# Kernel tuning notes

Measured on AMD Instinct MI355X. Metric: run time of the kernel, lower is better.

## Reference

```python
import jax, jax.numpy as jnp
import numpy as np

DIM, HID, SEQ = 768, 2048, 4096
LR, MOM, WD, THRESH = 1e-3, 0.9, 0.01, 0.1


def _net(p, x):
    W1, b1, W2, b2, W3, b3, W4, b4 = p
    h = jax.nn.relu(x @ W1 + b1)
    h = jax.nn.relu(h @ W2 + b2)
    h = jax.nn.relu(h @ W3 + b3)
    return h @ W4 + b4


def _loss(p, t):
    # t: [dim]; token.unsqueeze(0) then mse_loss (mean over all elements)
    pred = _net(p, t[None, :])
    return jnp.mean((pred - t[None, :]) ** 2)


def _ttt(params, x):
    toks = x[::4]  # `if i % 4 != 0: continue`

    def step(carry, t):
        p, buf, inited = carry
        g = jax.grad(_loss)(p, t)
        surprise = sum(jnp.linalg.norm(gi) for gi in jax.tree_util.tree_leaves(g))
        # momentum buffer: first observation initializes it
        buf_new = jnp.where(inited, MOM * buf + (1.0 - MOM) * surprise, surprise)

        def upd(q):
            qd = jax.tree_util.tree_map(lambda w: w * (1.0 - WD), q)  # weight decay
            g2 = jax.grad(_loss)(qd, t)                                # fresh fwd/bwd
            return jax.tree_util.tree_map(lambda w, gi: w - LR * gi, qd, g2)  # SGD step

        p_new = jax.lax.cond(buf_new > THRESH, upd, lambda q: q, p)
        return (p_new, buf_new, jnp.bool_(True)), None

    (pf, _, _), _ = jax.lax.scan(step, (params, jnp.float32(0.0), jnp.bool_(False)), toks)
    return pf


def setup_inputs() -> dict:
    key = jax.random.key(0)
    ks = jax.random.split(key, 5)

    def lin(k, fi, fo):
        kw, kb = jax.random.split(k)
        w = jax.random.normal(kw, (fi, fo), jnp.float32) / np.sqrt(fi).astype(np.float32)
        b = jax.random.normal(kb, (fo,), jnp.float32) * 0.01
        return w, b

    W1, b1 = lin(ks[0], DIM, HID)
    W2, b2 = lin(ks[1], HID, HID)
    W3, b3 = lin(ks[2], HID, HID)
    W4, b4 = lin(ks[3], HID, DIM)
    x = jax.random.normal(ks[4], (SEQ, DIM), jnp.float32)
    return dict(x=x, W1=W1, b1=b1, W2=W2, b2=b2, W3=W3, b3=b3, W4=W4, b4=b4, do_ttt=1)


def reference(x, W1, b1, W2, b2, W3, b3, W4, b4, do_ttt):
    params = (W1, b1, W2, b2, W3, b3, W4, b4)
    if do_ttt:
        params = _ttt(params, x)
    out = _net(params, x)            # eval pass over full sequence
    return out.mean(axis=0, keepdims=True)  # memory_summary [1, dim]
```

## Files before the change

### kernel.cpp

```cpp
#include <hip/hip_runtime.h>
#include <cstddef>

#define LRC 0.001f
#define DEC 0.99f

typedef float f32x4 __attribute__((ext_vector_type(4)));

static const size_t OFF_H1F = 376832;
static const size_t OFF_H2F = 380928;
static const size_t OFF_H2Q = 382976;
static const size_t OFF_H3F = 385024;
static const size_t OFF_H3Q = 387072;
static const size_t OFF_D4F = 389120;
static const size_t OFF_D4Q = 389888;
static const size_t OFF_D3F = 390656;
static const size_t OFF_D3Q = 392704;
static const size_t OFF_D2F = 394752;
static const size_t OFF_D2Q = 396800;
static const size_t OFF_SL4 = 398848;
static const size_t OFF_D1Q = 400896;
static const size_t OFF_NSQ = 402944;
static const size_t OFF_SL3 = 402960;
static const size_t OFF_SL2 = 403216;
static const size_t OFF_SL1 = 403472;
static const size_t OFF_MSUM = 403732;
static const size_t OFF_HA  = 428308;
static const size_t OFF_HB  = 2525460;

#define ST0  0
#define ST1  2048
#define ST2  4096
#define ST3  6144
#define SD4F 8192
#define SD4Q 8960
#define SRED 9728
#define SCND 10240
#define SBUF 10244
#define SCOND 10245
#define SB4  10248
#define SSQ  10256
#define SWRP 10264
#define SWRQ 10288

__device__ __forceinline__ float clf(const float* p) {
    return __hip_atomic_load(p, __ATOMIC_RELAXED, __HIP_MEMORY_SCOPE_AGENT);
}
__device__ __forceinline__ void csf(float* p, float v) {
    __hip_atomic_store(p, v, __ATOMIC_RELAXED, __HIP_MEMORY_SCOPE_AGENT);
}
__device__ __forceinline__ f32x4 cl4(const float* p) {
    f32x4 r;
    asm volatile("global_load_dwordx4 %0, %1, off sc0 sc1" : "=&v"(r) : "v"(p) : "memory");
    return r;
}
__device__ __forceinline__ void cs4(float* p, f32x4 v) {
    asm volatile("global_store_dwordx4 %0, %1, off sc0 sc1" :: "v"(p), "v"(v) : "memory");
}
__device__ __forceinline__ void vwait() {
    asm volatile("s_waitcnt vmcnt(0)" ::: "memory");
    __builtin_amdgcn_sched_barrier(0);
}

__device__ __forceinline__ float dot4(const f32x4 a, const f32x4 b) {
    float s = a.x * b.x; s += a.y * b.y; s += a.z * b.z; s += a.w * b.w; return s;
}
__device__ __forceinline__ int swz(int p) { return p ^ (((p >> 5) & 7) << 2); }

__device__ __forceinline__ void updc(f32x4& wv, const f32x4 a, float dq) {
    wv.x = DEC * wv.x - (LRC * a.x) * dq;
    wv.y = DEC * wv.y - (LRC * a.y) * dq;
    wv.z = DEC * wv.z - (LRC * a.z) * dq;
    wv.w = DEC * wv.w - (LRC * a.w) * dq;
}
__device__ __forceinline__ void updr(f32x4& wv, float u, const f32x4 dv) {
    wv.x = DEC * wv.x - u * dv.x;
    wv.y = DEC * wv.y - u * dv.y;
    wv.z = DEC * wv.z - u * dv.z;
    wv.w = DEC * wv.w - u * dv.w;
}

__device__ __forceinline__ float block_reduce_512s(float v, float* red) {
    int t = threadIdx.x;
    red[t] = v;
    __syncthreads();
    for (int st = 256; st > 0; st >>= 1) {
        if (t < st) red[t] += red[t + st];
        __syncthreads();
    }
    float r = red[0];
    __syncthreads();
    return r;
}

__device__ __forceinline__ void gbar(unsigned* bar) {
    asm volatile("s_waitcnt vmcnt(0) lgkmcnt(0)" ::: "memory");
    __syncthreads();
    if (threadIdx.x == 0) {
        unsigned g = __hip_atomic_load(bar, __ATOMIC_RELAXED, __HIP_MEMORY_SCOPE_AGENT);
        unsigned* grp = bar + 64 + ((blockIdx.x >> 4) << 5);
        bool released = false;
        if (__hip_atomic_fetch_add(grp, 1u, __ATOMIC_RELAXED, __HIP_MEMORY_SCOPE_AGENT) == 15u) {
            if (__hip_atomic_fetch_add(bar + 32, 1u, __ATOMIC_RELAXED, __HIP_MEMORY_SCOPE_AGENT) == 15u) {
#pragma unroll
                for (int i = 0; i < 16; ++i)
                    __hip_atomic_store(bar + 64 + (i << 5), 0u, __ATOMIC_RELAXED, __HIP_MEMORY_SCOPE_AGENT);
                __hip_atomic_store(bar + 32, 0u, __ATOMIC_RELAXED, __HIP_MEMORY_SCOPE_AGENT);
                __hip_atomic_store(bar, g + 1u, __ATOMIC_RELEASE, __HIP_MEMORY_SCOPE_AGENT);
                released = true;
            }
        }
        if (!released) {
            while (__hip_atomic_load(bar, __ATOMIC_RELAXED, __HIP_MEMORY_SCOPE_AGENT) == g)
                __builtin_amdgcn_s_sleep(2);
            (void)__hip_atomic_load(bar, __ATOMIC_ACQUIRE, __HIP_MEMORY_SCOPE_AGENT);
        }
    }
    __syncthreads();
}

__global__ __launch_bounds__(1024) void k_zero(unsigned* __restrict__ bar) {
    bar[threadIdx.x] = 0u;
}

#define L3M(M) M(0) M(1) M(2)
#define L8M(M) M(0) M(1) M(2) M(3) M(4) M(5) M(6) M(7)
#define LDS_SW(buf, i) (*(const f32x4*)(smem + (buf) + swz(32 * lane + 4 * (i))))
#define LDS_D4(buf, i) (*(const f32x4*)(smem + (buf) + 12 * lane + 4 * (i)))

__global__ void __attribute__((amdgpu_flat_work_group_size(512, 512), amdgpu_waves_per_eu(2, 2)))
k_scan(const float* __restrict__ x,
       float* __restrict__ W1g, float* __restrict__ b1g,
       float* __restrict__ W2g, float* __restrict__ b2g,
       float* __restrict__ W3g, float* __restrict__ b3g,
       float* __restrict__ W4g, float* __restrict__ b4g,
       float* __restrict__ wsf,
       const int* __restrict__ flag) {
    if (*flag == 0) return;
    __shared__ __align__(16) float smem[16896];
    unsigned* bar = (unsigned*)(wsf + OFF_HA);
    const int b = blockIdx.x, tid = threadIdx.x;
    const int w = tid >> 6, lane = tid & 63;
    const int jw = 8 * b + w;
    const int c3 = 3 * b;
    const int t4 = tid * 4;

    f32x4 w1c0, w1c1, w1c2;
    f32x4 w2c0, w2c1, w2c2, w2c3, w2c4, w2c5, w2c6, w2c7;
    f32x4 w3c0, w3c1, w3c2, w3c3, w3c4, w3c5, w3c6, w3c7;
    f32x4 w4c0, w4c1, w4c2;
    f32x4 w4r0, w4r1, w4r2;
    f32x4 w2r0, w2r1, w2r2, w2r3, w2r4, w2r5, w2r6, w2r7;
    f32x4 w3r0, w3r1, w3r2, w3r3, w3r4, w3r5, w3r6, w3r7;

#define LD_COL(dst, Wg, ld, row0, col) { f32x4 t; \
    t.x = Wg[(size_t)((row0) + 0) * (ld) + (col)]; \
    t.y = Wg[(size_t)((row0) + 1) * (ld) + (col)]; \
    t.z = Wg[(size_t)((row0) + 2) * (ld) + (col)]; \
    t.w = Wg[(size_t)((row0) + 3) * (ld) + (col)]; dst = t; }
#define LDW1C(i) LD_COL(w1c##i, W1g, 2048, 12 * lane + 4 * (i), jw)
    L3M(LDW1C)
#undef LDW1C
#define LDW2C(i) LD_COL(w2c##i, W2g, 2048, 32 * lane + 4 * (i), jw)
    L8M(LDW2C)
#undef LDW2C
#define LDW3C(i) LD_COL(w3c##i, W3g, 2048, 32 * lane + 4 * (i), jw)
    L8M(LDW3C)
#undef LDW3C
#define LDW4C(i) LD_COL(w4c##i, W4g, 768, 4 * tid, c3 + (i))
    L3M(LDW4C)
#undef LDW4C
#define LDW4R(i) w4r##i = *(const f32x4*)(W4g + (size_t)jw * 768 + 12 * lane + 4 * (i));
    L3M(LDW4R)
#undef LDW4R
#define LDW2R(i) w2r##i = *(const f32x4*)(W2g + (size_t)jw * 2048 + 32 * lane + 4 * (i));
    L8M(LDW2R)
#undef LDW2R
#define LDW3R(i) w3r##i = *(const f32x4*)(W3g + (size_t)jw * 2048 + 32 * lane + 4 * (i));
    L8M(LDW3R)
#undef LDW3R
    if (tid == 0) smem[SBUF] = 0.f;

    for (int s = 0; s < 1024; ++s) {
        const float* xt = x + (size_t)s * 3072;
        const float* xprev = x + (size_t)(s > 0 ? s - 1 : 0) * 3072;

        float cond = 0.f;
        if (s > 0) {
            if (w < 4) {
                const float* sl = wsf + (w == 0 ? OFF_SL1 : w == 1 ? OFF_SL2 : w == 2 ? OFF_SL3 : OFF_SL4);
                float v = clf(sl + lane) + clf(sl + lane + 64) + clf(sl + lane + 128) + clf(sl + lane + 192);
#pragma unroll
                for (int off = 32; off > 0; off >>= 1) v += __shfl_down(v, off);
                if (lane == 0) smem[SCND + w] = v;
            }
            __syncthreads();
            if (tid == 0) {
                float nd1 = sqrtf(smem[SCND + 0]), nd2 = sqrtf(smem[SCND + 1]);
                float nd3 = sqrtf(smem[SCND + 2]), nd4 = sqrtf(smem[SCND + 3]);
                float nx = sqrtf(clf(wsf + OFF_NSQ + 0));
                float nh1 = sqrtf(clf(wsf + OFF_NSQ + 1));
                float nh2 = sqrtf(clf(wsf + OFF_NSQ + 2));
                float nh3 = sqrtf(clf(wsf + OFF_NSQ + 3));
                float surprise = nx * nd1 + nd1 + nh1 * nd2 + nd2 + nh2 * nd3 + nd3 + nh3 * nd4 + nd4;
                float bufold = smem[SBUF];
                float bufnew = (s == 1) ? surprise : (0.9f * bufold + 0.1f * surprise);
                smem[SBUF] = bufnew;
                smem[SCOND] = (bufnew > 0.1f) ? 1.f : 0.f;
            }
            __syncthreads();
            cond = smem[SCOND];
        }
        float b1j;
        if (cond != 0.f) {
            f32x4 a0 = cl4(wsf + OFF_H1F + t4);
            f32x4 a1 = cl4(wsf + OFF_H2Q + t4);
            f32x4 a2 = cl4(wsf + OFF_D2Q + t4);
            f32x4 a3 = cl4(wsf + OFF_D3Q + t4);
            f32x4 hq3 = cl4(wsf + OFF_H3Q + t4);
            f32x4 d4s = {0.f, 0.f, 0.f, 0.f};
            if (tid < 192) d4s = cl4(wsf + OFF_D4Q + t4);
            float d1qj = clf(wsf + OFF_D1Q + jw);
            float h3qr = clf(wsf + OFF_H3Q + jw);
            float h2qr = clf(wsf + OFF_H2Q + jw);
            float ob1 = b1g[jw];
            f32x4 xp0 = *(const f32x4*)(xprev + 12 * lane);
            f32x4 xp1 = *(const f32x4*)(xprev + 12 * lane + 4);
            f32x4 xp2 = *(const f32x4*)(xprev + 12 * lane + 8);
            vwait();
            {
                int st = swz(t4);
                *(f32x4*)(smem + ST0 + st) = a0;
                *(f32x4*)(smem + ST1 + st) = a1;
                *(f32x4*)(smem + ST2 + st) = a2;
                *(f32x4*)(smem + ST3 + st) = a3;
            }
            if (tid < 192) *(f32x4*)(smem + SD4Q + t4) = d4s;
            __syncthreads();
            updc(w1c0, xp0, d1qj); updc(w1c1, xp1, d1qj); updc(w1c2, xp2, d1qj);
            {
                float d2qj = smem[ST2 + swz(jw)];
#define UPW2C(i) { f32x4 hf = LDS_SW(ST0, i); f32x4 af; \
                   af.x = DEC * hf.x; af.y = DEC * hf.y; af.z = DEC * hf.z; af.w = DEC * hf.w; \
                   updc(w2c##i, af, d2qj); }
                L8M(UPW2C)
#undef UPW2C
            }
            {
                float d3qj = smem[ST3 + swz(jw)];
#define UPW3C(i) { f32x4 hq = LDS_SW(ST1, i); updc(w3c##i, hq, d3qj); }
                L8M(UPW3C)
#undef UPW3C
            }
            {
                float vq0 = smem[SD4Q + c3 + 0];
                float vq1 = smem[SD4Q + c3 + 1];
                float vq2 = smem[SD4Q + c3 + 2];
                updc(w4c0, hq3, vq0); updc(w4c1, hq3, vq1); updc(w4c2, hq3, vq2);
            }
            {
                float u = LRC * h3qr;
#define UPW4R(i) { f32x4 dv = LDS_D4(SD4Q, i); updr(w4r##i, u, dv); }
                L3M(UPW4R)
#undef UPW4R
            }
            {
                float u = LRC * h2qr;
#define UPW3R(i) { f32x4 dv = LDS_SW(ST3, i); updr(w3r##i, u, dv); }
                L8M(UPW3R)
#undef UPW3R
            }
            {
                float u = LRC * (DEC * smem[ST0 + swz(jw)]);
#define UPW2R(i) { f32x4 dv = LDS_SW(ST2, i); updr(w2r##i, u, dv); }
                L8M(UPW2R)
#undef UPW2R
            }
            b1j = DEC * ob1 - LRC * d1qj;
            if (lane == 0) b1g[jw] = b1j;
        } else {
            b1j = b1g[jw];
        }
        {
            f32x4 x0 = *(const f32x4*)(xt + 12 * lane);
            f32x4 x1 = *(const f32x4*)(xt + 12 * lane + 4);
            f32x4 x2 = *(const f32x4*)(xt + 12 * lane + 8);
            float acc = dot4(w1c0, x0);
            acc += dot4(w1c1, x1);
            acc += dot4(w1c2, x2);
#pragma unroll
            for (int off = 32; off > 0; off >>= 1) acc += __shfl_down(acc, off);
            if (lane == 0) csf(wsf + OFF_H1F + jw, fmaxf(acc + b1j, 0.f));
        }
        gbar(bar);

        {
            f32x4 hv = cl4(wsf + OFF_H1F + t4);
            float ob2 = b2g[jw];
            float d2qjo = (cond != 0.f) ? clf(wsf + OFF_D2Q + jw) : 0.f;
            vwait();
            *(f32x4*)(smem + ST0 + swz(t4)) = hv;
            float b2j = (cond != 0.f) ? (DEC * ob2 - LRC * d2qjo) : ob2;
            if (cond != 0.f && lane == 0) b2g[jw] = b2j;
            __syncthreads();
            float accP = 0.f, accQ = 0.f;
#define PHB(i) { const f32x4 hf = LDS_SW(ST0, i); f32x4 hq; \
                 hq.x = DEC * hf.x; hq.y = DEC * hf.y; hq.z = DEC * hf.z; hq.w = DEC * hf.w; \
                 accP += dot4(w2c##i, hf); accQ += dot4(w2c##i, hq); }
            L8M(PHB)
#undef PHB
#pragma unroll
            for (int off = 32; off > 0; off >>= 1) {
                accP += __shfl_down(accP, off);
                accQ += __shfl_down(accQ, off);
            }
            if (lane == 0) {
                csf(wsf + OFF_H2F + jw, fmaxf(accP + b2j, 0.f));
                csf(wsf + OFF_H2Q + jw, fmaxf(DEC * (accQ + b2j), 0.f));
            }
        }
        gbar(bar);

        {
            f32x4 hfv = cl4(wsf + OFF_H2F + t4);
            f32x4 hqv = cl4(wsf + OFF_H2Q + t4);
            float ob3 = b3g[jw];
            float d3qjo = (cond != 0.f) ? clf(wsf + OFF_D3Q + jw) : 0.f;
            vwait();
            {
                int st = swz(t4);
                *(f32x4*)(smem + ST0 + st) = hfv;
                *(f32x4*)(smem + ST1 + st) = hqv;
            }
            float b3j = (cond != 0.f) ? (DEC * ob3 - LRC * d3qjo) : ob3;
            if (cond != 0.f && lane == 0) b3g[jw] = b3j;
            __syncthreads();
            float accP = 0.f, accQ = 0.f;
#define PHC(i) { const f32x4 hf = LDS_SW(ST0, i); const f32x4 hq = LDS_SW(ST1, i); \
                 accP += dot4(w3c##i, hf); accQ += dot4(w3c##i, hq); }
            L8M(PHC)
#undef PHC
#pragma unroll
            for (int off = 32; off > 0; off >>= 1) {
                accP += __shfl_down(accP, off);
                accQ += __shfl_down(accQ, off);
            }
            if (lane == 0) {
                csf(wsf + OFF_H3F + jw, fmaxf(accP + b3j, 0.f));
                csf(wsf + OFF_H3Q + jw, fmaxf(DEC * (accQ + b3j), 0.f));
            }
        }
        gbar(bar);

        {
            f32x4 hfv = cl4(wsf + OFF_H3F + t4);
            f32x4 hqv = cl4(wsf + OFF_H3Q + t4);
            float tv = 0.f;
            if (tid < 3) {
                float ob4 = b4g[c3 + tid];
                float d4qjo = (cond != 0.f) ? clf(wsf + OFF_D4Q + c3 + tid) : 0.f;
                tv = xt[c3 + tid];
                float bn = (cond != 0.f) ? (DEC * ob4 - LRC * d4qjo) : ob4;
                if (cond != 0.f) b4g[c3 + tid] = bn;
                smem[SB4 + tid] = bn;
            }
            vwait();
            {
                int st = swz(t4);
                *(f32x4*)(smem + ST0 + st) = hfv;
                *(f32x4*)(smem + ST1 + st) = hqv;
            }
            float aP0 = dot4(w4c0, hfv), aP1 = dot4(w4c1, hfv), aP2 = dot4(w4c2, hfv);
            float aQ0 = dot4(w4c0, hqv), aQ1 = dot4(w4c1, hqv), aQ2 = dot4(w4c2, hqv);
#pragma unroll
            for (int off = 32; off > 0; off >>= 1) {
                aP0 += __shfl_down(aP0, off); aP1 += __shfl_down(aP1, off); aP2 += __shfl_down(aP2, off);
                aQ0 += __shfl_down(aQ0, off); aQ1 += __shfl_down(aQ1, off); aQ2 += __shfl_down(aQ2, off);
            }
            if (lane == 0) {
                smem[SWRP + w * 3 + 0] = aP0; smem[SWRP + w * 3 + 1] = aP1; smem[SWRP + w * 3 + 2] = aP2;
                smem[SWRQ + w * 3 + 0] = aQ0; smem[SWRQ + w * 3 + 1] = aQ1; smem[SWRQ + w * 3 + 2] = aQ2;
            }
            __syncthreads();
            if (tid < 3) {
                float zp = 0.f, zq = 0.f;
#pragma unroll
                for (int q = 0; q < 8; ++q) { zp += smem[SWRP + q * 3 + tid]; zq += smem[SWRQ + q * 3 + tid]; }
                float bn = smem[SB4 + tid];
                float d4f = 2.f * ((zp + bn) - tv) * (1.f / 768.f);
                float d4q = 2.f * (DEC * (zq + bn) - tv) * (1.f / 768.f);
                csf(wsf + OFF_D4F + c3 + tid, d4f);
                csf(wsf + OFF_D4Q + c3 + tid, d4q);
                smem[SSQ + tid] = d4f * d4f;
            }
            __syncthreads();
            if (tid == 0) csf(wsf + OFF_SL4 + b, smem[SSQ + 0] + smem[SSQ + 1] + smem[SSQ + 2]);
            if (b >= 1 && b <= 4) {
                float v = 0.f;
                if (b == 4) {
                    if (tid < 192) {
                        f32x4 xv = *(const f32x4*)(xt + t4);
                        v = xv.x * xv.x + xv.y * xv.y + xv.z * xv.z + xv.w * xv.w;
                    }
                } else {
                    const float* src = (b == 1) ? wsf + OFF_H1F : (b == 2) ? wsf + OFF_H2F : wsf + OFF_H3F;
                    f32x4 hh = cl4(src + t4);
                    vwait();
                    v = hh.x * hh.x + hh.y * hh.y + hh.z * hh.z + hh.w * hh.w;
                }
                float sres = block_reduce_512s(v, smem + SRED);
                if (tid == 0) csf(wsf + OFF_NSQ + ((b == 4) ? 0 : b), sres);
            }
        }
        gbar(bar);

        {
            f32x4 p4 = {0.f, 0.f, 0.f, 0.f}, q4 = {0.f, 0.f, 0.f, 0.f};
            if (tid < 192) {
                p4 = cl4(wsf + OFF_D4F + t4);
                q4 = cl4(wsf + OFF_D4Q + t4);
            }
            vwait();
            if (tid < 192) {
                *(f32x4*)(smem + SD4F + t4) = p4;
                *(f32x4*)(smem + SD4Q + t4) = q4;
            }
            __syncthreads();
            float accP = 0.f, accQ = 0.f;
#define PHE(i) { const f32x4 dP = LDS_D4(SD4F, i); const f32x4 dQ = LDS_D4(SD4Q, i); \
                 accP += dot4(w4r##i, dP); accQ += dot4(w4r##i, dQ); }
            L3M(PHE)
#undef PHE
#pragma unroll
            for (int off = 32; off > 0; off >>= 1) {
                accP += __shfl_down(accP, off);
                accQ += __shfl_down(accQ, off);
            }
            if (lane == 0) {
                float dp = (smem[ST0 + swz(jw)] > 0.f) ? accP : 0.f;
                float dq = (smem[ST1 + swz(jw)] > 0.f) ? DEC * accQ : 0.f;
                csf(wsf + OFF_D3F + jw, dp);
                csf(wsf + OFF_D3Q + jw, dq);
                smem[SSQ + w] = dp * dp;
            }
            __syncthreads();
            if (tid == 0) {
                float ss = 0.f;
#pragma unroll
                for (int q = 0; q < 8; ++q) ss += smem[SSQ + q];
                csf(wsf + OFF_SL3 + b, ss);
            }
        }
        gbar(bar);

        {
            f32x4 fP = cl4(wsf + OFF_D3F + t4);
            f32x4 fQ = cl4(wsf + OFF_D3Q + t4);
            float h2fr = clf(wsf + OFF_H2F + jw);
            float h2qr = clf(wsf + OFF_H2Q + jw);
            vwait();
            {
                int st = swz(t4);
                *(f32x4*)(smem + ST2 + st) = fP;
                *(f32x4*)(smem + ST3 + st) = fQ;
            }
            __syncthreads();
            float accP = 0.f, accQ = 0.f;
#define PHF(i) { const f32x4 dP = LDS_SW(ST2, i); const f32x4 dQ = LDS_SW(ST3, i); \
                 accP += dot4(w3r##i, dP); accQ += dot4(w3r##i, dQ); }
            L8M(PHF)
#undef PHF
#pragma unroll
            for (int off = 32; off > 0; off >>= 1) {
                accP += __shfl_down(accP, off);
                accQ += __shfl_down(accQ, off);
            }
            if (lane == 0) {
                float dp = (h2fr > 0.f) ? accP : 0.f;
                float dq = (h2qr > 0.f) ? DEC * accQ : 0.f;
                csf(wsf + OFF_D2F + jw, dp);
                csf(wsf + OFF_D2Q + jw, dq);
                smem[SSQ + w] = dp * dp;
            }
            __syncthreads();
            if (tid == 0) {
                float ss = 0.f;
#pragma unroll
                for (int q = 0; q < 8; ++q) ss += smem[SSQ + q];
                csf(wsf + OFF_SL2 + b, ss);
            }
        }
        gbar(bar);

        {
            f32x4 fP = cl4(wsf + OFF_D2F + t4);
            f32x4 fQ = cl4(wsf + OFF_D2Q + t4);
            float h1fr = clf(wsf + OFF_H1F + jw);
            vwait();
            {
                int st = swz(t4);
                *(f32x4*)(smem + ST0 + st) = fP;
                *(f32x4*)(smem + ST1 + st) = fQ;
            }
            __syncthreads();
            float accP = 0.f, accQ = 0.f;
#define PHG(i) { const f32x4 dP = LDS_SW(ST0, i); const f32x4 dQ = LDS_SW(ST1, i); \
                 accP += dot4(w2r##i, dP); accQ += dot4(w2r##i, dQ); }
            L8M(PHG)
#undef PHG
#pragma unroll
            for (int off = 32; off > 0; off >>= 1) {
                accP += __shfl_down(accP, off);
                accQ += __shfl_down(accQ, off);
            }
            if (lane == 0) {
                float dp = (h1fr > 0.f) ? accP : 0.f;
                float h1qr = DEC * h1fr;
                float dq = (h1qr > 0.f) ? DEC * accQ : 0.f;
                csf(wsf + OFF_D1Q + jw, dq);
                smem[SSQ + w] = dp * dp;
            }
            __syncthreads();
            if (tid == 0) {
                float ss = 0.f;
#pragma unroll
                for (int q = 0; q < 8; ++q) ss += smem[SSQ + q];
                csf(wsf + OFF_SL1 + b, ss);
            }
        }
        gbar(bar);
    }

    {
        if (w < 4) {
            const float* sl = wsf + (w == 0 ? OFF_SL1 : w == 1 ? OFF_SL2 : w == 2 ? OFF_SL3 : OFF_SL4);
            float v = clf(sl + lane) + clf(sl + lane + 64) + clf(sl + lane + 128) + clf(sl + lane + 192);
#pragma unroll
            for (int off = 32; off > 0; off >>= 1) v += __shfl_down(v, off);
            if (lane == 0) smem[SCND + w] = v;
        }
        __syncthreads();
        if (tid == 0) {
            float nd1 = sqrtf(smem[SCND + 0]), nd2 = sqrtf(smem[SCND + 1]);
            float nd3 = sqrtf(smem[SCND + 2]), nd4 = sqrtf(smem[SCND + 3]);
            float nx = sqrtf(clf(wsf + OFF_NSQ + 0));
            float nh1 = sqrtf(clf(wsf + OFF_NSQ + 1));
            float nh2 = sqrtf(clf(wsf + OFF_NSQ + 2));
            float nh3 = sqrtf(clf(wsf + OFF_NSQ + 3));
            float surprise = nx * nd1 + nd1 + nh1 * nd2 + nd2 + nh2 * nd3 + nd3 + nh3 * nd4 + nd4;
            float bufnew = 0.9f * smem[SBUF] + 0.1f * surprise;
            smem[SCOND] = (bufnew > 0.1f) ? 1.f : 0.f;
        }
        __syncthreads();
        if (smem[SCOND] != 0.f) {
            const float* xpE = x + (size_t)1023 * 3072;
            f32x4 a0 = cl4(wsf + OFF_H1F + t4);
            f32x4 a1 = cl4(wsf + OFF_H2Q + t4);
            f32x4 hq3 = cl4(wsf + OFF_H3Q + t4);
            f32x4 d4s = {0.f, 0.f, 0.f, 0.f};
            if (tid < 192) d4s = cl4(wsf + OFF_D4Q + t4);
            float d1qj = clf(wsf + OFF_D1Q + jw);
            float d2qj = clf(wsf + OFF_D2Q + jw);
            float d3qj = clf(wsf + OFF_D3Q + jw);
            f32x4 xp0 = *(const f32x4*)(xpE + 12 * lane);
            f32x4 xp1 = *(const f32x4*)(xpE + 12 * lane + 4);
            f32x4 xp2 = *(const f32x4*)(xpE + 12 * lane + 8);
            vwait();
            {
                int st = swz(t4);
                *(f32x4*)(smem + ST0 + st) = a0;
                *(f32x4*)(smem + ST1 + st) = a1;
            }
            if (tid < 192) *(f32x4*)(smem + SD4Q + t4) = d4s;
            __syncthreads();
            updc(w1c0, xp0, d1qj); updc(w1c1, xp1, d1qj); updc(w1c2, xp2, d1qj);
#define EPW2C(i) { f32x4 hf = LDS_SW(ST0, i); f32x4 af; \
                   af.x = DEC * hf.x; af.y = DEC * hf.y; af.z = DEC * hf.z; af.w = DEC * hf.w; \
                   updc(w2c##i, af, d2qj); }
            L8M(EPW2C)
#undef EPW2C
#define EPW3C(i) { f32x4 hq = LDS_SW(ST1, i); updc(w3c##i, hq, d3qj); }
            L8M(EPW3C)
#undef EPW3C
            {
                float vq0 = smem[SD4Q + c3 + 0];
                float vq1 = smem[SD4Q + c3 + 1];
                float vq2 = smem[SD4Q + c3 + 2];
                updc(w4c0, hq3, vq0); updc(w4c1, hq3, vq1); updc(w4c2, hq3, vq2);
            }
            if (lane == 0) {
                b1g[jw] = DEC * b1g[jw] - LRC * d1qj;
                b2g[jw] = DEC * b2g[jw] - LRC * d2qj;
                b3g[jw] = DEC * b3g[jw] - LRC * d3qj;
            }
            if (tid < 3) b4g[c3 + tid] = DEC * b4g[c3 + tid] - LRC * smem[SD4Q + c3 + tid];
        }
    }

    __syncthreads();
    {
#define WBW2(i) { smem[(32 * lane + 4 * (i) + 0) * 8 + w] = w2c##i.x; \
                  smem[(32 * lane + 4 * (i) + 1) * 8 + w] = w2c##i.y; \
                  smem[(32 * lane + 4 * (i) + 2) * 8 + w] = w2c##i.z; \
                  smem[(32 * lane + 4 * (i) + 3) * 8 + w] = w2c##i.w; }
        L8M(WBW2)
#undef WBW2
        __syncthreads();
#pragma unroll
        for (int r2 = 0; r2 < 4; ++r2) {
            int r = t4 + r2;
            *(f32x4*)(W2g + (size_t)r * 2048 + 8 * b) = *(const f32x4*)(smem + r * 8);
            *(f32x4*)(W2g + (size_t)r * 2048 + 8 * b + 4) = *(const f32x4*)(smem + r * 8 + 4);
        }
        __syncthreads();
    }
    {
#define WBW3(i) { smem[(32 * lane + 4 * (i) + 0) * 8 + w] = w3c##i.x; \
                  smem[(32 * lane + 4 * (i) + 1) * 8 + w] = w3c##i.y; \
                  smem[(32 * lane + 4 * (i) + 2) * 8 + w] = w3c##i.z; \
                  smem[(32 * lane + 4 * (i) + 3) * 8 + w] = w3c##i.w; }
        L8M(WBW3)
#undef WBW3
        __syncthreads();
#pragma unroll
        for (int r2 = 0; r2 < 4; ++r2) {
            int r = t4 + r2;
            *(f32x4*)(W3g + (size_t)r * 2048 + 8 * b) = *(const f32x4*)(smem + r * 8);
            *(f32x4*)(W3g + (size_t)r * 2048 + 8 * b + 4) = *(const f32x4*)(smem + r * 8 + 4);
        }
        __syncthreads();
    }
    {
#define WBW1(i) { smem[(12 * lane + 4 * (i) + 0) * 8 + w] = w1c##i.x; \
                  smem[(12 * lane + 4 * (i) + 1) * 8 + w] = w1c##i.y; \
                  smem[(12 * lane + 4 * (i) + 2) * 8 + w] = w1c##i.z; \
                  smem[(12 * lane + 4 * (i) + 3) * 8 + w] = w1c##i.w; }
        L3M(WBW1)
#undef WBW1
        __syncthreads();
        for (int r = tid; r < 768; r += 512) {
            *(f32x4*)(W1g + (size_t)r * 2048 + 8 * b) = *(const f32x4*)(smem + r * 8);
            *(f32x4*)(W1g + (size_t)r * 2048 + 8 * b + 4) = *(const f32x4*)(smem + r * 8 + 4);
        }
        __syncthreads();
    }
    {
#define WBW4(c) { smem[(4 * tid + 0) * 3 + (c)] = w4c##c.x; \
                  smem[(4 * tid + 1) * 3 + (c)] = w4c##c.y; \
                  smem[(4 * tid + 2) * 3 + (c)] = w4c##c.z; \
                  smem[(4 * tid + 3) * 3 + (c)] = w4c##c.w; }
        L3M(WBW4)
#undef WBW4
        __syncthreads();
#pragma unroll
        for (int r2 = 0; r2 < 4; ++r2) {
            int r = t4 + r2;
            W4g[(size_t)r * 768 + c3 + 0] = smem[r * 3 + 0];
            W4g[(size_t)r * 768 + c3 + 1] = smem[r * 3 + 1];
            W4g[(size_t)r * 768 + c3 + 2] = smem[r * 3 + 2];
        }
    }
}

__global__ __launch_bounds__(256) void k_gemm(const float* __restrict__ A,
                                              const float* __restrict__ W,
                                              const float* __restrict__ bias,
                                              float* __restrict__ C,
                                              int M, int N, int K, int do_relu) {
    __shared__ float sA[16][64];
    __shared__ float sB[16][128];
    int bn = blockIdx.x, bm = blockIdx.y;
    int m0 = bm * 64, n0 = bn * 128;
    int tid = threadIdx.x;
    int tx = tid & 31, ty = tid >> 5;
    float acc[8][4];
#pragma unroll
    for (int i = 0; i < 8; ++i)
#pragma unroll
        for (int j = 0; j < 4; ++j) acc[i][j] = 0.f;

// ... 94 lines not shown
```

Baseline: 66.14 ms.

## Replicate published cross-block vectors into 8 copies to spread coherent reads

Every value a block publishes for other blocks (activations, deltas, norms, partial sums) is now written to 8 replica regions, and each block reads from the replica chosen by its block index mod 8. The aim is to spread the many coherent, cache-bypassing loads that all 256 blocks issue against the same small addresses after each grid barrier, reducing hot-spot contention on the same L2/memory channels. In exchange every publish costs 8 stores, and the barrier now waits for outstanding stores before arriving. The replicas reuse the workspace region at OFF_HB, which assumes that area is otherwise unused during the scan.

```diff
diff --git a/kernel.cpp b/kernel.cpp
--- a/kernel.cpp
+++ b/kernel.cpp
@@ -26,6 +26,7 @@
 static const size_t OFF_MSUM = 403732;
 static const size_t OFF_HA  = 428308;
 static const size_t OFF_HB  = 2525460;
+static const size_t OFF_STG = 2525460;
 
 #define ST0  0
 #define ST1  2048
@@ -53,12 +54,17 @@
     asm volatile("global_load_dwordx4 %0, %1, off sc0 sc1" : "=&v"(r) : "v"(p) : "memory");
     return r;
 }
-__device__ __forceinline__ void cs4(float* p, f32x4 v) {
-    asm volatile("global_store_dwordx4 %0, %1, off sc0 sc1" :: "v"(p), "v"(v) : "memory");
-}
 __device__ __forceinline__ void vwait() {
     asm volatile("s_waitcnt vmcnt(0)" ::: "memory");
     __builtin_amdgcn_sched_barrier(0);
+}
+
+__device__ __forceinline__ float* repb(float* wsf, int r) {
+    return (r == 0) ? wsf : (wsf + (OFF_STG - OFF_H1F) + (size_t)(r - 1) * 32768);
+}
+__device__ __forceinline__ void pubf(float* wsf, size_t off, float v) {
+#pragma unroll
+    for (int r = 0; r < 8; ++r) csf(repb(wsf, r) + off, v);
 }
 
 __device__ __forceinline__ float dot4(const f32x4 a, const f32x4 b) {
@@ -97,6 +103,7 @@
     __syncthreads();
     if (threadIdx.x == 0) {
         unsigned g = __hip_atomic_load(bar, __ATOMIC_RELAXED, __HIP_MEMORY_SCOPE_AGENT);
+        asm volatile("s_waitcnt vmcnt(0)" ::: "memory");
         unsigned* grp = bar + 64 + ((blockIdx.x >> 4) << 5);
         bool released = false;
         if (__hip_atomic_fetch_add(grp, 1u, __ATOMIC_RELAXED, __HIP_MEMORY_SCOPE_AGENT) == 15u) {
@@ -127,14 +134,14 @@
 #define LDS_SW(buf, i) (*(const f32x4*)(smem + (buf) + swz(32 * lane + 4 * (i))))
 #define LDS_D4(buf, i) (*(const f32x4*)(smem + (buf) + 12 * lane + 4 * (i)))
 
-__global__ void __attribute__((amdgpu_flat_work_group_size(512, 512), amdgpu_waves_per_eu(2, 2)))
-k_scan(const float* __restrict__ x,
-       float* __restrict__ W1g, float* __restrict__ b1g,
-       float* __restrict__ W2g, float* __restrict__ b2g,
-       float* __restrict__ W3g, float* __restrict__ b3g,
-       float* __restrict__ W4g, float* __restrict__ b4g,
-       float* __restrict__ wsf,
-       const int* __restrict__ flag) {
+__global__ __attribute__((amdgpu_flat_work_group_size(512, 512), amdgpu_waves_per_eu(2, 2)))
+void k_scan(const float* __restrict__ x,
+            float* __restrict__ W1g, float* __restrict__ b1g,
+            float* __restrict__ W2g, float* __restrict__ b2g,
+            float* __restrict__ W3g, float* __restrict__ b3g,
+            float* __restrict__ W4g, float* __restrict__ b4g,
+            float* __restrict__ wsf,
+            const int* __restrict__ flag) {
     if (*flag == 0) return;
     __shared__ __align__(16) float smem[16896];
     unsigned* bar = (unsigned*)(wsf + OFF_HA);
@@ -143,6 +150,7 @@
     const int jw = 8 * b + w;
     const int c3 = 3 * b;
     const int t4 = tid * 4;
+    float* rb = repb(wsf, b & 7);
 
     f32x4 w1c0, w1c1, w1c2;
     f32x4 w2c0, w2c1, w2c2, w2c3, w2c4, w2c5, w2c6, w2c7;
@@ -187,7 +195,7 @@
         float cond = 0.f;
         if (s > 0) {
             if (w < 4) {
-                const float* sl = wsf + (w == 0 ? OFF_SL1 : w == 1 ? OFF_SL2 : w == 2 ? OFF_SL3 : OFF_SL4);
+                const float* sl = rb + (w == 0 ? OFF_SL1 : w == 1 ? OFF_SL2 : w == 2 ? OFF_SL3 : OFF_SL4);
                 float v = clf(sl + lane) + clf(sl + lane + 64) + clf(sl + lane + 128) + clf(sl + lane + 192);
 #pragma unroll
                 for (int off = 32; off > 0; off >>= 1) v += __shfl_down(v, off);
@@ -197,10 +205,10 @@
             if (tid == 0) {
                 float nd1 = sqrtf(smem[SCND + 0]), nd2 = sqrtf(smem[SCND + 1]);
                 float nd3 = sqrtf(smem[SCND + 2]), nd4 = sqrtf(smem[SCND + 3]);
-                float nx = sqrtf(clf(wsf + OFF_NSQ + 0));
-                float nh1 = sqrtf(clf(wsf + OFF_NSQ + 1));
-                float nh2 = sqrtf(clf(wsf + OFF_NSQ + 2));
-                float nh3 = sqrtf(clf(wsf + OFF_NSQ + 3));
+                float nx = sqrtf(clf(rb + OFF_NSQ + 0));
+                float nh1 = sqrtf(clf(rb + OFF_NSQ + 1));
+                float nh2 = sqrtf(clf(rb + OFF_NSQ + 2));
+                float nh3 = sqrtf(clf(rb + OFF_NSQ + 3));
                 float surprise = nx * nd1 + nd1 + nh1 * nd2 + nd2 + nh2 * nd3 + nd3 + nh3 * nd4 + nd4;
                 float bufold = smem[SBUF];
                 float bufnew = (s == 1) ? surprise : (0.9f * bufold + 0.1f * surprise);
@@ -212,16 +220,16 @@
         }
         float b1j;
         if (cond != 0.f) {
-            f32x4 a0 = cl4(wsf + OFF_H1F + t4);
-            f32x4 a1 = cl4(wsf + OFF_H2Q + t4);
-            f32x4 a2 = cl4(wsf + OFF_D2Q + t4);
-            f32x4 a3 = cl4(wsf + OFF_D3Q + t4);
-            f32x4 hq3 = cl4(wsf + OFF_H3Q + t4);
+            f32x4 a0 = cl4(rb + OFF_H1F + t4);
+            f32x4 a1 = cl4(rb + OFF_H2Q + t4);
+            f32x4 a2 = cl4(rb + OFF_D2Q + t4);
+            f32x4 a3 = cl4(rb + OFF_D3Q + t4);
+            f32x4 hq3 = cl4(rb + OFF_H3Q + t4);
             f32x4 d4s = {0.f, 0.f, 0.f, 0.f};
-            if (tid < 192) d4s = cl4(wsf + OFF_D4Q + t4);
-            float d1qj = clf(wsf + OFF_D1Q + jw);
-            float h3qr = clf(wsf + OFF_H3Q + jw);
-            float h2qr = clf(wsf + OFF_H2Q + jw);
+            if (tid < 192) d4s = cl4(rb + OFF_D4Q + t4);
+            float d1qj = clf(rb + OFF_D1Q + jw);
+            float h3qr = clf(rb + OFF_H3Q + jw);
+            float h2qr = clf(rb + OFF_H2Q + jw);
             float ob1 = b1g[jw];
             f32x4 xp0 = *(const f32x4*)(xprev + 12 * lane);
             f32x4 xp1 = *(const f32x4*)(xprev + 12 * lane + 4);
@@ -289,14 +297,14 @@
             acc += dot4(w1c2, x2);
 #pragma unroll
             for (int off = 32; off > 0; off >>= 1) acc += __shfl_down(acc, off);
-            if (lane == 0) csf(wsf + OFF_H1F + jw, fmaxf(acc + b1j, 0.f));
+            if (lane == 0) pubf(wsf, OFF_H1F + jw, fmaxf(acc + b1j, 0.f));
         }
         gbar(bar);
 
         {
-            f32x4 hv = cl4(wsf + OFF_H1F + t4);
+            f32x4 hv = cl4(rb + OFF_H1F + t4);
             float ob2 = b2g[jw];
-            float d2qjo = (cond != 0.f) ? clf(wsf + OFF_D2Q + jw) : 0.f;
+            float d2qjo = (cond != 0.f) ? clf(rb + OFF_D2Q + jw) : 0.f;
             vwait();
             *(f32x4*)(smem + ST0 + swz(t4)) = hv;
             float b2j = (cond != 0.f) ? (DEC * ob2 - LRC * d2qjo) : ob2;
@@ -314,17 +322,17 @@
                 accQ += __shfl_down(accQ, off);
             }
             if (lane == 0) {
-                csf(wsf + OFF_H2F + jw, fmaxf(accP + b2j, 0.f));
-                csf(wsf + OFF_H2Q + jw, fmaxf(DEC * (accQ + b2j), 0.f));
+                pubf(wsf, OFF_H2F + jw, fmaxf(accP + b2j, 0.f));
+                pubf(wsf, OFF_H2Q + jw, fmaxf(DEC * (accQ + b2j), 0.f));
             }
         }
         gbar(bar);
 
         {
-            f32x4 hfv = cl4(wsf + OFF_H2F + t4);
-            f32x4 hqv = cl4(wsf + OFF_H2Q + t4);
+            f32x4 hfv = cl4(rb + OFF_H2F + t4);
+            f32x4 hqv = cl4(rb + OFF_H2Q + t4);
             float ob3 = b3g[jw];
-            float d3qjo = (cond != 0.f) ? clf(wsf + OFF_D3Q + jw) : 0.f;
+            float d3qjo = (cond != 0.f) ? clf(rb + OFF_D3Q + jw) : 0.f;
             vwait();
             {
                 int st = swz(t4);
@@ -345,19 +353,19 @@
                 accQ += __shfl_down(accQ, off);
             }
             if (lane == 0) {
-                csf(wsf + OFF_H3F + jw, fmaxf(accP + b3j, 0.f));
-                csf(wsf + OFF_H3Q + jw, fmaxf(DEC * (accQ + b3j), 0.f));
+                pubf(wsf, OFF_H3F + jw, fmaxf(accP + b3j, 0.f));
+                pubf(wsf, OFF_H3Q + jw, fmaxf(DEC * (accQ + b3j), 0.f));
             }
         }
         gbar(bar);
 
         {
-            f32x4 hfv = cl4(wsf + OFF_H3F + t4);
-            f32x4 hqv = cl4(wsf + OFF_H3Q + t4);
+            f32x4 hfv = cl4(rb + OFF_H3F + t4);
+            f32x4 hqv = cl4(rb + OFF_H3Q + t4);
             float tv = 0.f;
             if (tid < 3) {
                 float ob4 = b4g[c3 + tid];
-                float d4qjo = (cond != 0.f) ? clf(wsf + OFF_D4Q + c3 + tid) : 0.f;
+                float d4qjo = (cond != 0.f) ? clf(rb + OFF_D4Q + c3 + tid) : 0.f;
                 tv = xt[c3 + tid];
                 float bn = (cond != 0.f) ? (DEC * ob4 - LRC * d4qjo) : ob4;
                 if (cond != 0.f) b4g[c3 + tid] = bn;
@@ -388,12 +396,12 @@
                 float bn = smem[SB4 + tid];
                 float d4f = 2.f * ((zp + bn) - tv) * (1.f / 768.f);
                 float d4q = 2.f * (DEC * (zq + bn) - tv) * (1.f / 768.f);
-                csf(wsf + OFF_D4F + c3 + tid, d4f);
-                csf(wsf + OFF_D4Q + c3 + tid, d4q);
+                pubf(wsf, OFF_D4F + c3 + tid, d4f);
+                pubf(wsf, OFF_D4Q + c3 + tid, d4q);
                 smem[SSQ + tid] = d4f * d4f;
             }
             __syncthreads();
-            if (tid == 0) csf(wsf + OFF_SL4 + b, smem[SSQ + 0] + smem[SSQ + 1] + smem[SSQ + 2]);
+            if (tid == 0) pubf(wsf, OFF_SL4 + b, smem[SSQ + 0] + smem[SSQ + 1] + smem[SSQ + 2]);
             if (b >= 1 && b <= 4) {
                 float v = 0.f;
                 if (b == 4) {
@@ -402,13 +410,13 @@
                         v = xv.x * xv.x + xv.y * xv.y + xv.z * xv.z + xv.w * xv.w;
                     }
                 } else {
-                    const float* src = (b == 1) ? wsf + OFF_H1F : (b == 2) ? wsf + OFF_H2F : wsf + OFF_H3F;
-                    f32x4 hh = cl4(src + t4);
+                    const size_t soff = (b == 1) ? OFF_H1F : (b == 2) ? OFF_H2F : OFF_H3F;
+                    f32x4 hh = cl4(rb + soff + t4);
                     vwait();
                     v = hh.x * hh.x + hh.y * hh.y + hh.z * hh.z + hh.w * hh.w;
                 }
                 float sres = block_reduce_512s(v, smem + SRED);
-                if (tid == 0) csf(wsf + OFF_NSQ + ((b == 4) ? 0 : b), sres);
+                if (tid == 0) pubf(wsf, OFF_NSQ + ((b == 4) ? 0 : b), sres);
             }
         }
         gbar(bar);
@@ -416,8 +424,8 @@
         {
             f32x4 p4 = {0.f, 0.f, 0.f, 0.f}, q4 = {0.f, 0.f, 0.f, 0.f};
             if (tid < 192) {
-                p4 = cl4(wsf + OFF_D4F + t4);
-                q4 = cl4(wsf + OFF_D4Q + t4);
+                p4 = cl4(rb + OFF_D4F + t4);
+                q4 = cl4(rb + OFF_D4Q + t4);
             }
             vwait();
             if (tid < 192) {
@@ -438,8 +446,8 @@
             if (lane == 0) {
                 float dp = (smem[ST0 + swz(jw)] > 0.f) ? accP : 0.f;
                 float dq = (smem[ST1 + swz(jw)] > 0.f) ? DEC * accQ : 0.f;
-                csf(wsf + OFF_D3F + jw, dp);
-                csf(wsf + OFF_D3Q + jw, dq);
+                pubf(wsf, OFF_D3F + jw, dp);
+                pubf(wsf, OFF_D3Q + jw, dq);
                 smem[SSQ + w] = dp * dp;
             }
             __syncthreads();
@@ -447,16 +455,16 @@
                 float ss = 0.f;
 #pragma unroll
                 for (int q = 0; q < 8; ++q) ss += smem[SSQ + q];
-                csf(wsf + OFF_SL3 + b, ss);
+                pubf(wsf, OFF_SL3 + b, ss);
             }
         }
         gbar(bar);
 
         {
-            f32x4 fP = cl4(wsf + OFF_D3F + t4);
-            f32x4 fQ = cl4(wsf + OFF_D3Q + t4);
-            float h2fr = clf(wsf + OFF_H2F + jw);
-            float h2qr = clf(wsf + OFF_H2Q + jw);
+            f32x4 fP = cl4(rb + OFF_D3F + t4);
+            f32x4 fQ = cl4(rb + OFF_D3Q + t4);
+            float h2fr = clf(rb + OFF_H2F + jw);
+            float h2qr = clf(rb + OFF_H2Q + jw);
             vwait();
             {
                 int st = swz(t4);
@@ -477,8 +485,8 @@
             if (lane == 0) {
                 float dp = (h2fr > 0.f) ? accP : 0.f;
                 float dq = (h2qr > 0.f) ? DEC * accQ : 0.f;
-                csf(wsf + OFF_D2F + jw, dp);
-                csf(wsf + OFF_D2Q + jw, dq);
+                pubf(wsf, OFF_D2F + jw, dp);
+                pubf(wsf, OFF_D2Q + jw, dq);
                 smem[SSQ + w] = dp * dp;
             }
             __syncthreads();
@@ -486,15 +494,15 @@
                 float ss = 0.f;
 #pragma unroll
                 for (int q = 0; q < 8; ++q) ss += smem[SSQ + q];
-                csf(wsf + OFF_SL2 + b, ss);
+                pubf(wsf, OFF_SL2 + b, ss);
             }
         }
         gbar(bar);
 
         {
-            f32x4 fP = cl4(wsf + OFF_D2F + t4);
-            f32x4 fQ = cl4(wsf + OFF_D2Q + t4);
-            float h1fr = clf(wsf + OFF_H1F + jw);
+            f32x4 fP = cl4(rb + OFF_D2F + t4);
+            f32x4 fQ = cl4(rb + OFF_D2Q + t4);
+            float h1fr = clf(rb + OFF_H1F + jw);
             vwait();
             {
                 int st = swz(t4);
@@ -516,7 +524,7 @@
                 float dp = (h1fr > 0.f) ? accP : 0.f;
                 float h1qr = DEC * h1fr;
                 float dq = (h1qr > 0.f) ? DEC * accQ : 0.f;
-                csf(wsf + OFF_D1Q + jw, dq);
+                pubf(wsf, OFF_D1Q + jw, dq);
                 smem[SSQ + w] = dp * dp;
             }
             __syncthreads();
@@ -524,7 +532,7 @@
                 float ss = 0.f;
 #pragma unroll
                 for (int q = 0; q < 8; ++q) ss += smem[SSQ + q];
-                csf(wsf + OFF_SL1 + b, ss);
+                pubf(wsf, OFF_SL1 + b, ss);
             }
         }
         gbar(bar);
```

New measurement: 100.2 ms. 1.51x slower.

## Stage cross-block vectors into per-XCD L2 copies with local barriers

Applied to the files above, without the earlier changes.

After each grid barrier, blocks on the same XCD (found via HW_REG_XCC_ID) cooperatively copy the shared activation and delta vectors from coherent global memory into a per-XCD staging area. A local barrier then lets every block read them with sc0-only loads that may hit the local L2, instead of each block doing system-coherent sc0 sc1 loads. The aim is to cut repeated cross-die coherent traffic on every scan step. The cost is an extra copy and an extra per-XCD barrier at each phase, plus reliance on the XCD id mapping and cache semantics for correctness.

```diff
diff --git a/kernel.cpp b/kernel.cpp
--- a/kernel.cpp
+++ b/kernel.cpp
@@ -26,6 +26,7 @@
 static const size_t OFF_MSUM = 403732;
 static const size_t OFF_HA  = 428308;
 static const size_t OFF_HB  = 2525460;
+static const size_t OFF_STG = 2525460;
 
 #define ST0  0
 #define ST1  2048
@@ -53,12 +54,20 @@
     asm volatile("global_load_dwordx4 %0, %1, off sc0 sc1" : "=&v"(r) : "v"(p) : "memory");
     return r;
 }
-__device__ __forceinline__ void cs4(float* p, f32x4 v) {
-    asm volatile("global_store_dwordx4 %0, %1, off sc0 sc1" :: "v"(p), "v"(v) : "memory");
-}
 __device__ __forceinline__ void vwait() {
     asm volatile("s_waitcnt vmcnt(0)" ::: "memory");
     __builtin_amdgcn_sched_barrier(0);
+}
+__device__ __forceinline__ f32x4 s4(const float* p) {
+    f32x4 r;
+    asm volatile("global_load_dwordx4 %0, %1, off sc0" : "=&v"(r) : "v"(p) : "memory");
+    return r;
+}
+__device__ __forceinline__ float s1(const float* p) {
+    float r;
+    asm volatile("global_load_dword %0, %1, off sc0\n\t"
+                 "s_waitcnt vmcnt(0)" : "=&v"(r) : "v"(p) : "memory");
+    return r;
 }
 
 __device__ __forceinline__ float dot4(const f32x4 a, const f32x4 b) {
@@ -97,6 +106,7 @@
     __syncthreads();
     if (threadIdx.x == 0) {
         unsigned g = __hip_atomic_load(bar, __ATOMIC_RELAXED, __HIP_MEMORY_SCOPE_AGENT);
+        asm volatile("s_waitcnt vmcnt(0)" ::: "memory");
         unsigned* grp = bar + 64 + ((blockIdx.x >> 4) << 5);
         bool released = false;
         if (__hip_atomic_fetch_add(grp, 1u, __ATOMIC_RELAXED, __HIP_MEMORY_SCOPE_AGENT) == 15u) {
@@ -118,8 +128,40 @@
     __syncthreads();
 }
 
+__device__ __forceinline__ void lbar(unsigned* lg, unsigned* la, unsigned m) {
+    asm volatile("s_waitcnt vmcnt(0) lgkmcnt(0)" ::: "memory");
+    __syncthreads();
+    if (threadIdx.x == 0) {
+        unsigned g = __hip_atomic_load(lg, __ATOMIC_RELAXED, __HIP_MEMORY_SCOPE_AGENT);
+        asm volatile("s_waitcnt vmcnt(0)" ::: "memory");
+        if (__hip_atomic_fetch_add(la, 1u, __ATOMIC_RELAXED, __HIP_MEMORY_SCOPE_AGENT) == m - 1u) {
+            __hip_atomic_store(la, 0u, __ATOMIC_RELAXED, __HIP_MEMORY_SCOPE_AGENT);
+            __hip_atomic_store(lg, g + 1u, __ATOMIC_RELEASE, __HIP_MEMORY_SCOPE_AGENT);
+        } else {
+            while (__hip_atomic_load(lg, __ATOMIC_RELAXED, __HIP_MEMORY_SCOPE_AGENT) == g)
+                __builtin_amdgcn_s_sleep(1);
+            (void)__hip_atomic_load(lg, __ATOMIC_ACQUIRE, __HIP_MEMORY_SCOPE_AGENT);
+        }
+    }
+    __syncthreads();
+}
+
+__device__ __forceinline__ void scpy1(const float* src, float* dst, unsigned n4,
+                                      unsigned rank, unsigned m, int tid) {
+    unsigned c = rank + m * (unsigned)tid;
+    if (c < n4) {
+        f32x4 v;
+        asm volatile("global_load_dwordx4 %0, %1, off sc0 sc1\n\t"
+                     "s_waitcnt vmcnt(0)"
+                     : "=&v"(v) : "v"(src + 4u * c) : "memory");
+        asm volatile("global_store_dwordx4 %0, %1, off sc0"
+                     :: "v"(dst + 4u * c), "v"(v) : "memory");
+    }
+}
+
 __global__ __launch_bounds__(1024) void k_zero(unsigned* __restrict__ bar) {
-    bar[threadIdx.x] = 0u;
+    int t = threadIdx.x;
+    bar[t] = 0u; bar[t + 1024] = 0u; bar[t + 2048] = 0u; bar[t + 3072] = 0u;
 }
 
 #define L3M(M) M(0) M(1) M(2)
@@ -127,14 +169,14 @@
 #define LDS_SW(buf, i) (*(const f32x4*)(smem + (buf) + swz(32 * lane + 4 * (i))))
 #define LDS_D4(buf, i) (*(const f32x4*)(smem + (buf) + 12 * lane + 4 * (i)))
 
-__global__ void __attribute__((amdgpu_flat_work_group_size(512, 512), amdgpu_waves_per_eu(2, 2)))
-k_scan(const float* __restrict__ x,
-       float* __restrict__ W1g, float* __restrict__ b1g,
-       float* __restrict__ W2g, float* __restrict__ b2g,
-       float* __restrict__ W3g, float* __restrict__ b3g,
-       float* __restrict__ W4g, float* __restrict__ b4g,
-       float* __restrict__ wsf,
-       const int* __restrict__ flag) {
+__global__ __attribute__((amdgpu_flat_work_group_size(512, 512), amdgpu_waves_per_eu(2, 2)))
+void k_scan(const float* __restrict__ x,
+            float* __restrict__ W1g, float* __restrict__ b1g,
+            float* __restrict__ W2g, float* __restrict__ b2g,
+            float* __restrict__ W3g, float* __restrict__ b3g,
+            float* __restrict__ W4g, float* __restrict__ b4g,
+            float* __restrict__ wsf,
+            const int* __restrict__ flag) {
     if (*flag == 0) return;
     __shared__ __align__(16) float smem[16896];
     unsigned* bar = (unsigned*)(wsf + OFF_HA);
@@ -143,6 +185,22 @@
     const int jw = 8 * b + w;
     const int c3 = 3 * b;
     const int t4 = tid * 4;
+
+    unsigned xcc;
+    asm volatile("s_getreg_b32 %0, hwreg(HW_REG_XCC_ID)" : "=s"(xcc));
+    xcc &= 7u;
+    unsigned* cns  = bar + 1024 + xcc * 16;
+    unsigned* lgen = bar + 2048 + xcc * 16;
+    unsigned* larr = bar + 3072 + xcc * 16;
+    float* stg = wsf + (OFF_STG - OFF_H1F) + (size_t)xcc * 32768;
+    unsigned* smU = (unsigned*)smem;
+    if (tid == 0) smU[0] = __hip_atomic_fetch_add(cns, 1u, __ATOMIC_RELAXED, __HIP_MEMORY_SCOPE_AGENT);
+    gbar(bar);
+    if (tid == 0) smU[1] = __hip_atomic_load(cns, __ATOMIC_RELAXED, __HIP_MEMORY_SCOPE_AGENT);
+    __syncthreads();
+    const unsigned rank = smU[0];
+    const unsigned m = smU[1];
+    __syncthreads();
 
     f32x4 w1c0, w1c1, w1c2;
     f32x4 w2c0, w2c1, w2c2, w2c3, w2c4, w2c5, w2c6, w2c7;
@@ -184,11 +242,15 @@
         const float* xt = x + (size_t)s * 3072;
         const float* xprev = x + (size_t)(s > 0 ? s - 1 : 0) * 3072;
 
+        scpy1(wsf + OFF_D1Q, stg + OFF_D1Q, 512, rank, m, tid);
+        scpy1(wsf + OFF_NSQ, stg + OFF_NSQ, 196, rank, m, tid);
+        scpy1(wsf + OFF_SL4, stg + OFF_SL4, 64, rank, m, tid);
+        lbar(lgen, larr, m);
         float cond = 0.f;
         if (s > 0) {
             if (w < 4) {
-                const float* sl = wsf + (w == 0 ? OFF_SL1 : w == 1 ? OFF_SL2 : w == 2 ? OFF_SL3 : OFF_SL4);
-                float v = clf(sl + lane) + clf(sl + lane + 64) + clf(sl + lane + 128) + clf(sl + lane + 192);
+                const float* sl = stg + (w == 0 ? OFF_SL1 : w == 1 ? OFF_SL2 : w == 2 ? OFF_SL3 : OFF_SL4);
+                float v = s1(sl + lane) + s1(sl + lane + 64) + s1(sl + lane + 128) + s1(sl + lane + 192);
 #pragma unroll
                 for (int off = 32; off > 0; off >>= 1) v += __shfl_down(v, off);
                 if (lane == 0) smem[SCND + w] = v;
@@ -197,10 +259,10 @@
             if (tid == 0) {
                 float nd1 = sqrtf(smem[SCND + 0]), nd2 = sqrtf(smem[SCND + 1]);
                 float nd3 = sqrtf(smem[SCND + 2]), nd4 = sqrtf(smem[SCND + 3]);
-                float nx = sqrtf(clf(wsf + OFF_NSQ + 0));
-                float nh1 = sqrtf(clf(wsf + OFF_NSQ + 1));
-                float nh2 = sqrtf(clf(wsf + OFF_NSQ + 2));
-                float nh3 = sqrtf(clf(wsf + OFF_NSQ + 3));
+                float nx = sqrtf(s1(stg + OFF_NSQ + 0));
+                float nh1 = sqrtf(s1(stg + OFF_NSQ + 1));
+                float nh2 = sqrtf(s1(stg + OFF_NSQ + 2));
+                float nh3 = sqrtf(s1(stg + OFF_NSQ + 3));
                 float surprise = nx * nd1 + nd1 + nh1 * nd2 + nd2 + nh2 * nd3 + nd3 + nh3 * nd4 + nd4;
                 float bufold = smem[SBUF];
                 float bufnew = (s == 1) ? surprise : (0.9f * bufold + 0.1f * surprise);
@@ -212,16 +274,16 @@
         }
         float b1j;
         if (cond != 0.f) {
-            f32x4 a0 = cl4(wsf + OFF_H1F + t4);
-            f32x4 a1 = cl4(wsf + OFF_H2Q + t4);
-            f32x4 a2 = cl4(wsf + OFF_D2Q + t4);
-            f32x4 a3 = cl4(wsf + OFF_D3Q + t4);
-            f32x4 hq3 = cl4(wsf + OFF_H3Q + t4);
+            f32x4 a0 = s4(stg + OFF_H1F + t4);
+            f32x4 a1 = s4(stg + OFF_H2Q + t4);
+            f32x4 a2 = s4(stg + OFF_D2Q + t4);
+            f32x4 a3 = s4(stg + OFF_D3Q + t4);
+            f32x4 hq3 = s4(stg + OFF_H3Q + t4);
             f32x4 d4s = {0.f, 0.f, 0.f, 0.f};
-            if (tid < 192) d4s = cl4(wsf + OFF_D4Q + t4);
-            float d1qj = clf(wsf + OFF_D1Q + jw);
-            float h3qr = clf(wsf + OFF_H3Q + jw);
-            float h2qr = clf(wsf + OFF_H2Q + jw);
+            if (tid < 192) d4s = s4(stg + OFF_D4Q + t4);
+            float d1qj = s1(stg + OFF_D1Q + jw);
+            float h3qr = s1(stg + OFF_H3Q + jw);
+            float h2qr = s1(stg + OFF_H2Q + jw);
             float ob1 = b1g[jw];
             f32x4 xp0 = *(const f32x4*)(xprev + 12 * lane);
             f32x4 xp1 = *(const f32x4*)(xprev + 12 * lane + 4);
@@ -294,9 +356,11 @@
         gbar(bar);
 
         {
-            f32x4 hv = cl4(wsf + OFF_H1F + t4);
+            scpy1(wsf + OFF_H1F, stg + OFF_H1F, 512, rank, m, tid);
+            lbar(lgen, larr, m);
+            f32x4 hv = s4(stg + OFF_H1F + t4);
             float ob2 = b2g[jw];
-            float d2qjo = (cond != 0.f) ? clf(wsf + OFF_D2Q + jw) : 0.f;
+            float d2qjo = (cond != 0.f) ? s1(stg + OFF_D2Q + jw) : 0.f;
             vwait();
             *(f32x4*)(smem + ST0 + swz(t4)) = hv;
             float b2j = (cond != 0.f) ? (DEC * ob2 - LRC * d2qjo) : ob2;
@@ -321,10 +385,13 @@
         gbar(bar);
 
         {
-            f32x4 hfv = cl4(wsf + OFF_H2F + t4);
-            f32x4 hqv = cl4(wsf + OFF_H2Q + t4);
+            scpy1(wsf + OFF_H2F, stg + OFF_H2F, 512, rank, m, tid);
+            scpy1(wsf + OFF_H2Q, stg + OFF_H2Q, 512, rank, m, tid);
+            lbar(lgen, larr, m);
+            f32x4 hfv = s4(stg + OFF_H2F + t4);
+            f32x4 hqv = s4(stg + OFF_H2Q + t4);
             float ob3 = b3g[jw];
-            float d3qjo = (cond != 0.f) ? clf(wsf + OFF_D3Q + jw) : 0.f;
+            float d3qjo = (cond != 0.f) ? s1(stg + OFF_D3Q + jw) : 0.f;
             vwait();
             {
                 int st = swz(t4);
@@ -352,12 +419,15 @@
         gbar(bar);
 
         {
-            f32x4 hfv = cl4(wsf + OFF_H3F + t4);
-            f32x4 hqv = cl4(wsf + OFF_H3Q + t4);
+            scpy1(wsf + OFF_H3F, stg + OFF_H3F, 512, rank, m, tid);
+            scpy1(wsf + OFF_H3Q, stg + OFF_H3Q, 512, rank, m, tid);
+            lbar(lgen, larr, m);
+            f32x4 hfv = s4(stg + OFF_H3F + t4);
+            f32x4 hqv = s4(stg + OFF_H3Q + t4);
             float tv = 0.f;
             if (tid < 3) {
                 float ob4 = b4g[c3 + tid];
-                float d4qjo = (cond != 0.f) ? clf(wsf + OFF_D4Q + c3 + tid) : 0.f;
+                float d4qjo = (cond != 0.f) ? s1(stg + OFF_D4Q + c3 + tid) : 0.f;
                 tv = xt[c3 + tid];
                 float bn = (cond != 0.f) ? (DEC * ob4 - LRC * d4qjo) : ob4;
                 if (cond != 0.f) b4g[c3 + tid] = bn;
@@ -402,8 +472,8 @@
                         v = xv.x * xv.x + xv.y * xv.y + xv.z * xv.z + xv.w * xv.w;
                     }
                 } else {
-                    const float* src = (b == 1) ? wsf + OFF_H1F : (b == 2) ? wsf + OFF_H2F : wsf + OFF_H3F;
-                    f32x4 hh = cl4(src + t4);
+                    const size_t soff = (b == 1) ? OFF_H1F : (b == 2) ? OFF_H2F : OFF_H3F;
+                    f32x4 hh = s4(stg + soff + t4);
                     vwait();
                     v = hh.x * hh.x + hh.y * hh.y + hh.z * hh.z + hh.w * hh.w;
                 }
@@ -414,10 +484,13 @@
         gbar(bar);
 
         {
+            scpy1(wsf + OFF_D4F, stg + OFF_D4F, 192, rank, m, tid);
+            scpy1(wsf + OFF_D4Q, stg + OFF_D4Q, 192, rank, m, tid);
+            lbar(lgen, larr, m);
             f32x4 p4 = {0.f, 0.f, 0.f, 0.f}, q4 = {0.f, 0.f, 0.f, 0.f};
             if (tid < 192) {
-                p4 = cl4(wsf + OFF_D4F + t4);
-                q4 = cl4(wsf + OFF_D4Q + t4);
+                p4 = s4(stg + OFF_D4F + t4);
+                q4 = s4(stg + OFF_D4Q + t4);
             }
             vwait();
             if (tid < 192) {
@@ -453,10 +526,13 @@
         gbar(bar);
 
         {
-            f32x4 fP = cl4(wsf + OFF_D3F + t4);
-            f32x4 fQ = cl4(wsf + OFF_D3Q + t4);
-            float h2fr = clf(wsf + OFF_H2F + jw);
-            float h2qr = clf(wsf + OFF_H2Q + jw);
+            scpy1(wsf + OFF_D3F, stg + OFF_D3F, 512, rank, m, tid);
+            scpy1(wsf + OFF_D3Q, stg + OFF_D3Q, 512, rank, m, tid);
+            lbar(lgen, larr, m);
+            f32x4 fP = s4(stg + OFF_D3F + t4);
+            f32x4 fQ = s4(stg + OFF_D3Q + t4);
+            float h2fr = s1(stg + OFF_H2F + jw);
+            float h2qr = s1(stg + OFF_H2Q + jw);
             vwait();
             {
                 int st = swz(t4);
@@ -492,9 +568,12 @@
         gbar(bar);
 
         {
-            f32x4 fP = cl4(wsf + OFF_D2F + t4);
-            f32x4 fQ = cl4(wsf + OFF_D2Q + t4);
-            float h1fr = clf(wsf + OFF_H1F + jw);
+            scpy1(wsf + OFF_D2F, stg + OFF_D2F, 512, rank, m, tid);
+            scpy1(wsf + OFF_D2Q, stg + OFF_D2Q, 512, rank, m, tid);
+            lbar(lgen, larr, m);
+            f32x4 fP = s4(stg + OFF_D2F + t4);
+            f32x4 fQ = s4(stg + OFF_D2Q + t4);
+            float h1fr = s1(stg + OFF_H1F + jw);
             vwait();
             {
                 int st = swz(t4);
```

Result: slower. 106.7 ms (+61.3%).
